# Kernel tuning notes

Measured on AMD Instinct MI355X. Metric: run time of the kernel, lower is better.

## Reference

```python
import jax, jax.numpy as jnp
import numpy as np

N = 100000   # nodes
E = 1600000  # edges
IN = 128     # in_dim
HID = 64     # hidden_dim per head
H = 4        # heads
OUT = 2      # out_dim (classes)
HD = HID * H # 256
NEG_SLOPE = 0.2
BN_EPS = 1e-5


def setup_inputs() -> dict:
    key = jax.random.key(0)
    ks = jax.random.split(key, 24)
    rn = lambda k, shp, s=0.05: (jax.random.normal(k, shp, jnp.float32) * s)
    d = {}
    d['x'] = jax.random.normal(ks[0], (N, IN), jnp.float32)
    d['edge_index'] = jax.random.randint(ks[1], (2, E), 0, N, dtype=jnp.int64)
    # layer 0: 128 -> (4,64)
    d['W0'] = rn(ks[2], (IN, HD))
    d['a_src0'] = rn(ks[3], (H, HID), 0.1)
    d['a_dst0'] = rn(ks[4], (H, HID), 0.1)
    d['b0'] = jnp.zeros((HD,), jnp.float32)
    # layer 1: 256 -> (4,64)
    d['W1'] = rn(ks[5], (HD, HD))
    d['a_src1'] = rn(ks[6], (H, HID), 0.1)
    d['a_dst1'] = rn(ks[7], (H, HID), 0.1)
    d['b1'] = jnp.zeros((HD,), jnp.float32)
    # layer 2: 256 -> (1,2), concat=False
    d['W2'] = rn(ks[8], (HD, OUT))
    d['a_src2'] = rn(ks[9], (1, OUT), 0.1)
    d['a_dst2'] = rn(ks[10], (1, OUT), 0.1)
    d['b2'] = jnp.zeros((OUT,), jnp.float32)
    # skip projection for layer 0 (128 != 256)
    d['skipW'] = rn(ks[11], (IN, HD))
    d['skipb'] = jnp.zeros((HD,), jnp.float32)
    # batchnorm affine params
    d['g0'] = jnp.ones((HD,), jnp.float32); d['be0'] = jnp.zeros((HD,), jnp.float32)
    d['g1'] = jnp.ones((HD,), jnp.float32); d['be1'] = jnp.zeros((HD,), jnp.float32)
    d['g2'] = jnp.ones((OUT,), jnp.float32); d['be2'] = jnp.zeros((OUT,), jnp.float32)
    return d


def _gat_conv(x, src, dst, W, a_src, a_dst, b, heads, ch, concat):
    n = x.shape[0]
    h = (x @ W).reshape(n, heads, ch)                 # [N,H,C]
    alpha_src = jnp.sum(h * a_src, axis=-1)           # [N,H]
    alpha_dst = jnp.sum(h * a_dst, axis=-1)           # [N,H]
    e = alpha_src[src] + alpha_dst[dst]               # [E',H]
    e = jax.nn.leaky_relu(e, NEG_SLOPE)
    # segment softmax over incoming edges of each dst node
    m = jax.ops.segment_max(e, dst, num_segments=n)
    e = jnp.exp(e - m[dst])
    s = jax.ops.segment_sum(e, dst, num_segments=n)
    alpha = e / (s[dst] + 1e-16)                      # [E',H]
    out = jax.ops.segment_sum(h[src] * alpha[..., None], dst, num_segments=n)  # [N,H,C]
    out = out.reshape(n, heads * ch) if concat else out.mean(axis=1)
    return out + b


def _bn(x, g, b):
    mu = x.mean(axis=0)
    v = x.var(axis=0)  # biased, matches torch BN training normalization
    return g * (x - mu) * jax.lax.rsqrt(v + BN_EPS) + b


def reference(x, edge_index, W0, a_src0, a_dst0, b0, W1, a_src1, a_dst1, b1,
              W2, a_src2, a_dst2, b2, skipW, skipb, g0, be0, g1, be1, g2, be2):
    n = x.shape[0]
    loop = jnp.arange(n, dtype=edge_index.dtype)
    src = jnp.concatenate([edge_index[0], loop])  # self-loops (PyG default)
    dst = jnp.concatenate([edge_index[1], loop])

    residual = x
    # layer 0
    h = _gat_conv(x, src, dst, W0, a_src0, a_dst0, b0, H, HID, True)
    h = _bn(h, g0, be0)
    h = h + (residual @ skipW + skipb)
    residual = h
    h = jax.nn.elu(h)
    # layer 1
    h = _gat_conv(h, src, dst, W1, a_src1, a_dst1, b1, H, HID, True)
    h = _bn(h, g1, be1)
    h = h + residual  # Identity skip
    h = jax.nn.elu(h)
    # layer 2 (heads=1, concat=False)
    h = _gat_conv(h, src, dst, W2, a_src2, a_dst2, b2, 1, OUT, False)
    h = _bn(h, g2, be2)
    return h
```

## Files before the change

kernel.cpp:

```cpp
#include <hip/hip_runtime.h>
#include <cstdint>
#include <cstddef>

#define KN 100000
#define KE 1600000
#define KE2 (KE + KN)
#define KIN 128
#define KHD 256
#define KH 4

#define BSH 7
#define NBUK ((KN + 127) >> 7)
#define BCAP 2560
#define ACHUNK 8192

#define LRELU(x) ((x) > 0.f ? (x) : 0.2f * (x))

typedef unsigned short bfu;
typedef short bf16x8 __attribute__((ext_vector_type(8)));
typedef unsigned short u16x8 __attribute__((ext_vector_type(8)));
typedef float f32x4 __attribute__((ext_vector_type(4)));

__device__ __forceinline__ float bf2f(bfu u) {
    union { unsigned int i; float f; } c; c.i = ((unsigned int)u) << 16; return c.f;
}
__device__ __forceinline__ bfu f2bf(float f) {
    union { float f; unsigned int i; } c; c.f = f;
    unsigned int r = c.i + 0x7FFFu + ((c.i >> 16) & 1u);
    return (bfu)(r >> 16);
}
__device__ __forceinline__ float eluf(float x) { return x > 0.f ? x : expm1f(x); }

__global__ __launch_bounds__(256) void k_binA(const int* __restrict__ ei,
                                              int* __restrict__ gcur,
                                              uint2* __restrict__ stg) {
    __shared__ int cnt[NBUK];
    __shared__ int base[NBUK];
    int t = threadIdx.x;
    for (int i = t; i < NBUK; i += 256) cnt[i] = 0;
    __syncthreads();
    int e0 = blockIdx.x * ACHUNK;
    int rank[ACHUNK / 256];
#pragma unroll
    for (int i = 0; i < ACHUNK / 256; ++i) {
        int e = e0 + i * 256 + t;
        rank[i] = 0;
        if (e < KE2) {
            int d = (e < KE) ? ei[KE + e] : (e - KE);
            rank[i] = atomicAdd(&cnt[d >> BSH], 1);
        }
    }
    __syncthreads();
    for (int b = t; b < NBUK; b += 256) {
        int c = cnt[b];
        base[b] = c ? atomicAdd(&gcur[b], c) : 0;
    }
    __syncthreads();
#pragma unroll
    for (int i = 0; i < ACHUNK / 256; ++i) {
        int e = e0 + i * 256 + t;
        if (e < KE2) {
            int d = (e < KE) ? ei[KE + e] : (e - KE);
            int s = (e < KE) ? ei[e] : (e - KE);
            int b = d >> BSH;
            int pos = base[b] + rank[i];
            if (pos < BCAP) stg[(size_t)b * BCAP + pos] = make_uint2((unsigned)s, (unsigned)d);
        }
    }
}

__global__ __launch_bounds__(1024) void k_scanB(const int* __restrict__ gcur,
                                                int* __restrict__ gbase,
                                                int* __restrict__ rowptr) {
    __shared__ int s[1024];
    int t = threadIdx.x;
    int v = (t < NBUK) ? min(gcur[t], BCAP) : 0;
    s[t] = v;
    __syncthreads();
    for (int o = 1; o < 1024; o <<= 1) {
        int add = (t >= o) ? s[t - o] : 0;
        __syncthreads();
        s[t] += add;
        __syncthreads();
    }
    if (t < NBUK) gbase[t] = s[t] - v;
    if (t == 0) rowptr[KN] = KE2;
}

__global__ __launch_bounds__(256) void k_binB(const int* __restrict__ gcur,
                                              const int* __restrict__ gbase,
                                              const uint2* __restrict__ stg,
                                              int* __restrict__ rowptr,
                                              int* __restrict__ csrc) {
    __shared__ int lcnt[128];
    __shared__ int lcur[128];
    __shared__ int ss[128];
    __shared__ int loff[128];
    int b = blockIdx.x, t = threadIdx.x;
    if (t < 128) { lcnt[t] = 0; lcur[t] = 0; }
    __syncthreads();
    int n = min(gcur[b], BCAP);
    int node0 = b << BSH;
    const uint2* sp = stg + (size_t)b * BCAP;
    for (int i = t; i < n; i += 256) {
        int d = (int)sp[i].y;
        atomicAdd(&lcnt[d - node0], 1);
    }
    __syncthreads();
    int v = (t < 128) ? lcnt[t] : 0;
    if (t < 128) ss[t] = v;
    __syncthreads();
    for (int o = 1; o < 128; o <<= 1) {
        int add = (t < 128 && t >= o) ? ss[t - o] : 0;
        __syncthreads();
        if (t < 128) ss[t] += add;
        __syncthreads();
    }
    int gb = gbase[b];
    if (t < 128) {
        loff[t] = ss[t] - v;
        int node = node0 + t;
        if (node < KN) rowptr[node] = gb + ss[t] - v;
    }
    __syncthreads();
    for (int i = t; i < n; i += 256) {
        uint2 r = sp[i];
        int li = (int)r.y - node0;
        int rank = atomicAdd(&lcur[li], 1);
        csrc[gb + loff[li] + rank] = (int)r.x;
    }
}

__global__ void k_cvt_w(const float* __restrict__ W, bfu* __restrict__ Wt, int K) {
    int t = blockIdx.x * 256 + threadIdx.x;
    if (t >= K * 256) return;
    int n = t & 255;
    int k = t >> 8;
    Wt[(size_t)n * K + k] = f2bf(W[(size_t)k * 256 + n]);
}

__global__ __launch_bounds__(256) void k_mgemm_dual(const float* __restrict__ Ap,
                                                    const bfu* __restrict__ Wcat,
                                                    const float* __restrict__ skipb,
                                                    bfu* __restrict__ hout,
                                                    bfu* __restrict__ sout, int M,
                                                    const float* __restrict__ avs,
                                                    const float* __restrict__ avd,
                                                    float* __restrict__ as_out,
                                                    float* __restrict__ ad_out) {
    const int K = KIN;
    __shared__ bfu As[128 * 40];
    __shared__ bfu Bs[128 * 40];
    int t = threadIdx.x;
    int row0 = blockIdx.x * 128;
    int col0 = blockIdx.y * 128;
    int srow = t >> 1;
    int shalf = t & 1;
    int l = t & 63;
    int w = t >> 6;
    int wr = w >> 1, wc = w & 1;
    int lg = l >> 4, lm = l & 15;

    f32x4 acc[4][4] = {};

    for (int kk = 0; kk < K; kk += 32) {
        {
            int garow = row0 + srow;
            bfu abuf[16];
            if (garow < M) {
                const float* ap = Ap + (size_t)garow * K + kk + shalf * 16;
#pragma unroll
                for (int i = 0; i < 4; ++i) {
                    float4 v = ((const float4*)ap)[i];
                    abuf[i * 4 + 0] = f2bf(v.x); abuf[i * 4 + 1] = f2bf(v.y);
                    abuf[i * 4 + 2] = f2bf(v.z); abuf[i * 4 + 3] = f2bf(v.w);
                }
            } else {
#pragma unroll
                for (int i = 0; i < 16; ++i) abuf[i] = 0;
            }
            *(u16x8*)(&As[srow * 40 + shalf * 16]) = *(const u16x8*)(&abuf[0]);
            *(u16x8*)(&As[srow * 40 + shalf * 16 + 8]) = *(const u16x8*)(&abuf[8]);
        }
        {
            const bfu* bp = Wcat + (size_t)(col0 + srow) * K + kk + shalf * 16;
            *(u16x8*)(&Bs[srow * 40 + shalf * 16]) = *(const u16x8*)bp;
            *(u16x8*)(&Bs[srow * 40 + shalf * 16 + 8]) = *(const u16x8*)(bp + 8);
        }
        __syncthreads();
        {
            int a_base = (wr * 64 + lm) * 40 + lg * 8;
            int b_base = (wc * 64 + lm) * 40 + lg * 8;
            bf16x8 af[4], bf_[4];
#pragma unroll
            for (int m = 0; m < 4; ++m) af[m] = *(const bf16x8*)(&As[a_base + m * 16 * 40]);
#pragma unroll
            for (int n = 0; n < 4; ++n) bf_[n] = *(const bf16x8*)(&Bs[b_base + n * 16 * 40]);
#pragma unroll
            for (int m = 0; m < 4; ++m)
#pragma unroll
                for (int n = 0; n < 4; ++n)
                    acc[m][n] = __builtin_amdgcn_mfma_f32_16x16x32_bf16(af[m], bf_[n], acc[m][n], 0, 0, 0);
        }
        __syncthreads();
    }

    bool isH = (blockIdx.y < 2);
    if (isH) {
        int head = (blockIdx.y << 1) + wc;
        const float* ah_s = avs + head * 64;
        const float* ah_d = avd + head * 64;
        float wsv[4], wdv[4];
#pragma unroll
        for (int n = 0; n < 4; ++n) {
            wsv[n] = ah_s[n * 16 + lm];
            wdv[n] = ah_d[n * 16 + lm];
        }
#pragma unroll
        for (int m = 0; m < 4; ++m) {
#pragma unroll
            for (int r = 0; r < 4; ++r) {
                float ps = 0.f, pd = 0.f;
#pragma unroll
                for (int n = 0; n < 4; ++n) {
                    float v = acc[m][n][r];
                    ps += v * wsv[n];
                    pd += v * wdv[n];
                }
#pragma unroll
                for (int off = 1; off < 16; off <<= 1) {
                    ps += __shfl_xor(ps, off, 16);
                    pd += __shfl_xor(pd, off, 16);
                }
                int rrow = row0 + wr * 64 + m * 16 + lg * 4 + r;
                if (lm == 0 && rrow < M) {
                    as_out[rrow * 4 + head] = ps;
                    ad_out[rrow * 4 + head] = pd;
                }
            }
        }
    }

    bfu* outp = isH ? hout : sout;
    int ocol = (isH ? col0 : col0 - 256) + wc * 64 + lm;
    float bv[4];
#pragma unroll
    for (int n = 0; n < 4; ++n)
        bv[n] = isH ? 0.f : skipb[ocol + n * 16];
#pragma unroll
    for (int m = 0; m < 4; ++m) {
#pragma unroll
        for (int r = 0; r < 4; ++r) {
            int rrow = row0 + wr * 64 + m * 16 + lg * 4 + r;
            if (rrow < M) {
                size_t base = (size_t)rrow * 256 + ocol;
#pragma unroll
                for (int n = 0; n < 4; ++n)
                    outp[base + n * 16] = f2bf(acc[m][n][r] + bv[n]);
            }
        }
    }
}

__global__ __launch_bounds__(256) void k_mgemm1(const bfu* __restrict__ Ap,
                                                const bfu* __restrict__ Wt,
                                                bfu* __restrict__ Cout, int M,
                                                const float* __restrict__ avs,
                                                const float* __restrict__ avd,
                                                float* __restrict__ as_out,
                                                float* __restrict__ ad_out) {
    const int K = KHD;
    __shared__ bfu As[128 * 40];
    __shared__ bfu Bs[128 * 40];
    int t = threadIdx.x;
    int row0 = blockIdx.x * 128;
    int col0 = blockIdx.y * 128;
    int srow = t >> 1;
    int shalf = t & 1;
    int l = t & 63;
    int w = t >> 6;
    int wr = w >> 1, wc = w & 1;
    int lg = l >> 4, lm = l & 15;

    f32x4 acc[4][4] = {};

    for (int kk = 0; kk < K; kk += 32) {
        {
            int garow = row0 + srow;
            bfu abuf[16];
            if (garow < M) {
                const bfu* ap = Ap + (size_t)garow * K + kk + shalf * 16;
                u16x8 u0 = *(const u16x8*)ap;
                u16x8 u1 = *(const u16x8*)(ap + 8);
#pragma unroll
                for (int i = 0; i < 8; ++i) abuf[i] = f2bf(eluf(bf2f(u0[i])));
#pragma unroll
                for (int i = 0; i < 8; ++i) abuf[8 + i] = f2bf(eluf(bf2f(u1[i])));
            } else {
#pragma unroll
                for (int i = 0; i < 16; ++i) abuf[i] = 0;
            }
            *(u16x8*)(&As[srow * 40 + shalf * 16]) = *(const u16x8*)(&abuf[0]);
            *(u16x8*)(&As[srow * 40 + shalf * 16 + 8]) = *(const u16x8*)(&abuf[8]);
        }
        {
            const bfu* bp = Wt + (size_t)(col0 + srow) * K + kk + shalf * 16;
            *(u16x8*)(&Bs[srow * 40 + shalf * 16]) = *(const u16x8*)bp;
            *(u16x8*)(&Bs[srow * 40 + shalf * 16 + 8]) = *(const u16x8*)(bp + 8);
        }
        __syncthreads();
        {
            int a_base = (wr * 64 + lm) * 40 + lg * 8;
            int b_base = (wc * 64 + lm) * 40 + lg * 8;
            bf16x8 af[4], bf_[4];
#pragma unroll
            for (int m = 0; m < 4; ++m) af[m] = *(const bf16x8*)(&As[a_base + m * 16 * 40]);
#pragma unroll
            for (int n = 0; n < 4; ++n) bf_[n] = *(const bf16x8*)(&Bs[b_base + n * 16 * 40]);
#pragma unroll
            for (int m = 0; m < 4; ++m)
#pragma unroll
                for (int n = 0; n < 4; ++n)
                    acc[m][n] = __builtin_amdgcn_mfma_f32_16x16x32_bf16(af[m], bf_[n], acc[m][n], 0, 0, 0);
        }
        __syncthreads();
    }

    {
        int head = (blockIdx.y << 1) + wc;
        const float* ah_s = avs + head * 64;
        const float* ah_d = avd + head * 64;
        float wsv[4], wdv[4];
#pragma unroll
        for (int n = 0; n < 4; ++n) {
            wsv[n] = ah_s[n * 16 + lm];
            wdv[n] = ah_d[n * 16 + lm];
        }
#pragma unroll
        for (int m = 0; m < 4; ++m) {
#pragma unroll
            for (int r = 0; r < 4; ++r) {
                float ps = 0.f, pd = 0.f;
#pragma unroll
                for (int n = 0; n < 4; ++n) {
                    float v = acc[m][n][r];
                    ps += v * wsv[n];
                    pd += v * wdv[n];
                }
#pragma unroll
                for (int off = 1; off < 16; off <<= 1) {
                    ps += __shfl_xor(ps, off, 16);
                    pd += __shfl_xor(pd, off, 16);
                }
                int rrow = row0 + wr * 64 + m * 16 + lg * 4 + r;
                if (lm == 0 && rrow < M) {
                    as_out[rrow * 4 + head] = ps;
                    ad_out[rrow * 4 + head] = pd;
                }
            }
        }
    }

#pragma unroll
    for (int m = 0; m < 4; ++m) {
#pragma unroll
        for (int r = 0; r < 4; ++r) {
            int rrow = row0 + wr * 64 + m * 16 + lg * 4 + r;
            if (rrow < M) {
                size_t base = (size_t)rrow * 256 + col0 + wc * 64 + lm;
#pragma unroll
                for (int n = 0; n < 4; ++n)
                    Cout[base + n * 16] = f2bf(acc[m][n][r] + 0.f);
            }
        }
    }
}

__global__ __launch_bounds__(256) void k_gat_agg(const bfu* __restrict__ h,
                                                 const int* __restrict__ rowptr,
                                                 const int* __restrict__ csrc,
                                                 const float* __restrict__ asrc,
                                                 const float* __restrict__ adst,
                                                 const float* __restrict__ bias,
                                                 bfu* __restrict__ outb) {
    int wave = threadIdx.x >> 6, lane = threadIdx.x & 63;
    int node = blockIdx.x * 4 + wave;
    if (node >= KN) return;
    int p0 = rowptr[node], p1 = rowptr[node + 1];
    int head = lane >> 4;
    int c0 = lane << 2;
    float adh = adst[node * 4 + head];

    float sum = 0.f, a0 = 0.f, a1 = 0.f, a2 = 0.f, a3 = 0.f;
    int p = p0;
    while (p < p1 && (p & 3)) {
        int s = csrc[p];
        float e = asrc[s * 4 + head] + adh; e = LRELU(e);
        float w = __expf(e);
        ushort4 u = *(const ushort4*)(h + (size_t)s * 256 + c0);
        a0 += bf2f(u.x) * w; a1 += bf2f(u.y) * w;
        a2 += bf2f(u.z) * w; a3 += bf2f(u.w) * w;
        sum += w;
        ++p;
    }
    for (; p + 7 < p1; p += 8) {
        int4 ca = *(const int4*)(csrc + p);
        int4 cb = *(const int4*)(csrc + p + 4);
        int sx[8] = {ca.x, ca.y, ca.z, ca.w, cb.x, cb.y, cb.z, cb.w};
        ushort4 u[8];
#pragma unroll
        for (int j = 0; j < 8; ++j)
            u[j] = *(const ushort4*)(h + (size_t)sx[j] * 256 + c0);
        float wv[8];
#pragma unroll
        for (int j = 0; j < 8; ++j) {
            float e = asrc[sx[j] * 4 + head] + adh; e = LRELU(e);
            wv[j] = __expf(e);
        }
#pragma unroll
        for (int j = 0; j < 8; ++j) {
            a0 += bf2f(u[j].x) * wv[j];
            a1 += bf2f(u[j].y) * wv[j];
            a2 += bf2f(u[j].z) * wv[j];
            a3 += bf2f(u[j].w) * wv[j];
            sum += wv[j];
        }
    }
    for (; p + 3 < p1; p += 4) {
        int4 ca = *(const int4*)(csrc + p);
        int sx[4] = {ca.x, ca.y, ca.z, ca.w};
        ushort4 u[4];
#pragma unroll
        for (int j = 0; j < 4; ++j)
            u[j] = *(const ushort4*)(h + (size_t)sx[j] * 256 + c0);
#pragma unroll
        for (int j = 0; j < 4; ++j) {
            float e = asrc[sx[j] * 4 + head] + adh; e = LRELU(e);
            float w = __expf(e);
            a0 += bf2f(u[j].x) * w; a1 += bf2f(u[j].y) * w;
            a2 += bf2f(u[j].z) * w; a3 += bf2f(u[j].w) * w;
            sum += w;
        }
    }
    for (; p < p1; ++p) {
        int s = csrc[p];
        float e = asrc[s * 4 + head] + adh; e = LRELU(e);
        float w = __expf(e);
        ushort4 u = *(const ushort4*)(h + (size_t)s * 256 + c0);
        a0 += bf2f(u.x) * w; a1 += bf2f(u.y) * w;
        a2 += bf2f(u.z) * w; a3 += bf2f(u.w) * w;
        sum += w;
    }
    float inv = 1.f / (sum + 1e-16f);
    float4 bv = *(const float4*)(bias + c0);
    ushort4 o;
    o.x = f2bf(a0 * inv + bv.x);
    o.y = f2bf(a1 * inv + bv.y);
    o.z = f2bf(a2 * inv + bv.z);
    o.w = f2bf(a3 * inv + bv.w);
    *(ushort4*)(outb + (size_t)node * 256 + c0) = o;
}

__global__ __launch_bounds__(256) void k_bn_stats(const bfu* __restrict__ xx,
                                                  float* __restrict__ sums,
                                                  float* __restrict__ sumsq) {
    int t = threadIdx.x;
    float s = 0.f, q = 0.f;
    for (int row = blockIdx.x; row < KN; row += gridDim.x) {
        float v = bf2f(xx[(size_t)row * 256 + t]);
        s += v; q += v * v;
    }
    atomicAdd(&sums[t], s);
    atomicAdd(&sumsq[t], q);
}

__global__ void k_bn_params(const float* __restrict__ sums, const float* __restrict__ sumsq,
                            const float* __restrict__ g, const float* __restrict__ be,
                            float* __restrict__ scaleC, float* __restrict__ shiftC) {
    int c = threadIdx.x;
    float mean = sums[c] / (float)KN;
    float var = sumsq[c] / (float)KN - mean * mean;
    float inv = rsqrtf(var + 1e-5f);
    float sc = g[c] * inv;
    scaleC[c] = sc;
    shiftC[c] = be[c] - mean * sc;
}

__global__ __launch_bounds__(256) void k_finalize_skip(bfu* __restrict__ P,
                                                       const bfu* __restrict__ skipQ,
                                                       const float* __restrict__ scaleC,
                                                       const float* __restrict__ shiftC) {
    size_t i = ((size_t)blockIdx.x * 256 + threadIdx.x) * 8;
    int c0 = (int)(i & 255);
    u16x8 pv = *(const u16x8*)(P + i);
    u16x8 qv = *(const u16x8*)(skipQ + i);
    float4 s0 = *(const float4*)(scaleC + c0);
    float4 s1 = *(const float4*)(scaleC + c0 + 4);
    float4 h0 = *(const float4*)(shiftC + c0);
    float4 h1 = *(const float4*)(shiftC + c0 + 4);
    float sc[8] = {s0.x, s0.y, s0.z, s0.w, s1.x, s1.y, s1.z, s1.w};
    float sh[8] = {h0.x, h0.y, h0.z, h0.w, h1.x, h1.y, h1.z, h1.w};
    u16x8 o;
#pragma unroll
    for (int j = 0; j < 8; ++j) {
        float r = bf2f(pv[j]) * sc[j] + sh[j] + bf2f(qv[j]);
        o[j] = f2bf(r);
    }
    *(u16x8*)(P + i) = o;
}

__global__ __launch_bounds__(256) void k_finalize_add(const bfu* __restrict__ Q,
                                                      bfu* __restrict__ P,
                                                      const float* __restrict__ scaleC,
                                                      const float* __restrict__ shiftC) {
    size_t i = ((size_t)blockIdx.x * 256 + threadIdx.x) * 8;
    int c0 = (int)(i & 255);
    u16x8 qv = *(const u16x8*)(Q + i);
    u16x8 pv = *(const u16x8*)(P + i);
    float4 s0 = *(const float4*)(scaleC + c0);
    float4 s1 = *(const float4*)(scaleC + c0 + 4);
    float4 h0 = *(const float4*)(shiftC + c0);
    float4 h1 = *(const float4*)(shiftC + c0 + 4);
    float sc[8] = {s0.x, s0.y, s0.z, s0.w, s1.x, s1.y, s1.z, s1.w};
    float sh[8] = {h0.x, h0.y, h0.z, h0.w, h1.x, h1.y, h1.z, h1.w};
    u16x8 o;
#pragma unroll
    for (int j = 0; j < 8; ++j) {
        float r = bf2f(qv[j]) * sc[j] + sh[j] + bf2f(pv[j]);
        o[j] = f2bf(eluf(r));
    }
    *(u16x8*)(P + i) = o;
}

__global__ __launch_bounds__(256) void k_gemm2(const bfu* __restrict__ xx,
                                               const float* __restrict__ W,
                                               const float* __restrict__ as2,
                                               const float* __restrict__ ad2,
                                               float* __restrict__ h2,
                                               float* __restrict__ asrc,
                                               float* __restrict__ adst) {
    int lane = threadIdx.x & 63;
    int wid = blockIdx.x * 4 + (threadIdx.x >> 6);
    int c = lane * 4;
    float2 w0 = *(const float2*)(W + 2 * (c + 0));
    float2 w1 = *(const float2*)(W + 2 * (c + 1));
    float2 w2 = *(const float2*)(W + 2 * (c + 2));
    float2 w3 = *(const float2*)(W + 2 * (c + 3));
    float s0 = as2[0], s1 = as2[1], d0 = ad2[0], d1 = ad2[1];
    int nwaves = gridDim.x * 4;
    for (int node = wid; node < KN; node += nwaves) {
        ushort4 u = *(const ushort4*)(xx + (size_t)node * 256 + c);
        float v0 = bf2f(u.x), v1 = bf2f(u.y), v2 = bf2f(u.z), v3 = bf2f(u.w);
        float a0 = v0 * w0.x + v1 * w1.x + v2 * w2.x + v3 * w3.x;
        float a1 = v0 * w0.y + v1 * w1.y + v2 * w2.y + v3 * w3.y;
        for (int o = 32; o > 0; o >>= 1) {
            a0 += __shfl_down(a0, o);
            a1 += __shfl_down(a1, o);
        }
        if (lane == 0) {
            h2[2 * node] = a0; h2[2 * node + 1] = a1;
            asrc[node] = a0 * s0 + a1 * s1;
            adst[node] = a0 * d0 + a1 * d1;
        }
    }
}

__global__ void k_gat_agg2(const float* __restrict__ h2, const int* __restrict__ rowptr,
                           const int* __restrict__ csrc, const float* __restrict__ asrc,
                           const float* __restrict__ adst, const float* __restrict__ b2,
                           float* __restrict__ agg2) {
    int node = blockIdx.x * blockDim.x + threadIdx.x;
    if (node >= KN) return;
    int p0 = rowptr[node], p1 = rowptr[node + 1];
    float ad = adst[node];
    float sum = 0.f, acc0 = 0.f, acc1 = 0.f;
    int p = p0;
    for (; p + 1 < p1; p += 2) {
        int s0 = csrc[p], s1 = csrc[p + 1];
        float e0 = asrc[s0] + ad; e0 = LRELU(e0);
        float e1 = asrc[s1] + ad; e1 = LRELU(e1);
        float w0 = __expf(e0), w1 = __expf(e1);
        float2 v0 = *(const float2*)(h2 + 2 * s0);
        float2 v1 = *(const float2*)(h2 + 2 * s1);
        acc0 += w0 * v0.x + w1 * v1.x;
        acc1 += w0 * v0.y + w1 * v1.y;
        sum += w0 + w1;
    }
    if (p < p1) {
        int s = csrc[p];
        float e = asrc[s] + ad; e = LRELU(e);
        float w = __expf(e);
        float2 v = *(const float2*)(h2 + 2 * s);
        acc0 += w * v.x; acc1 += w * v.y;
        sum += w;
    }
    float inv = 1.f / (sum + 1e-16f);
    agg2[2 * node] = acc0 * inv + b2[0];
    agg2[2 * node + 1] = acc1 * inv + b2[1];
}

__global__ __launch_bounds__(256) void k_bn_stats2(const float* __restrict__ xx,
                                                   float* __restrict__ st) {
    int t = threadIdx.x;
    float s0 = 0, q0 = 0, s1 = 0, q1 = 0;
    for (int i = blockIdx.x * 256 + t; i < KN; i += gridDim.x * 256) {
        float v0 = xx[2 * i], v1 = xx[2 * i + 1];
        s0 += v0; q0 += v0 * v0; s1 += v1; q1 += v1 * v1;
    }
    for (int o = 32; o > 0; o >>= 1) {
        s0 += __shfl_down(s0, o); q0 += __shfl_down(q0, o);
        s1 += __shfl_down(s1, o); q1 += __shfl_down(q1, o);
    }
    __shared__ float red[4][4];
    int lane = t & 63, wv = t >> 6;
    if (lane == 0) { red[wv][0] = s0; red[wv][1] = q0; red[wv][2] = s1; red[wv][3] = q1; }
    __syncthreads();
    if (t == 0) {
        float a = 0, b = 0, c = 0, d = 0;
        for (int w = 0; w < 4; ++w) { a += red[w][0]; b += red[w][1]; c += red[w][2]; d += red[w][3]; }
        atomicAdd(&st[0], a); atomicAdd(&st[1], b); atomicAdd(&st[2], c); atomicAdd(&st[3], d);
    }
}

__global__ void k_finalize2(const float* __restrict__ agg2, const float* __restrict__ st,
                            const float* __restrict__ g, const float* __restrict__ be,
                            float* __restrict__ outp) {
    int i = blockIdx.x * blockDim.x + threadIdx.x;
    if (i >= 2 * KN) return;
    int c = i & 1;
    float mean = st[c * 2] / (float)KN;
    float var = st[c * 2 + 1] / (float)KN - mean * mean;
    float inv = rsqrtf(var + 1e-5f);
    outp[i] = (agg2[i] - mean) * g[c] * inv + be[c];
}

extern "C" void kernel_launch(void* const* d_in, const int* in_sizes, int n_in,
                              void* d_out, int out_size, void* d_ws, size_t ws_size,
                              hipStream_t stream) {
    (void)in_sizes; (void)n_in; (void)out_size; (void)ws_size;
    const float* x     = (const float*)d_in[0];
    const int*   ei    = (const int*)d_in[1];
    const float* W0    = (const float*)d_in[2];
    const float* as0   = (const float*)d_in[3];
    const float* ad0   = (const float*)d_in[4];
    const float* b0    = (const float*)d_in[5];
    const float* W1    = (const float*)d_in[6];
    const float* as1   = (const float*)d_in[7];
    const float* ad1   = (const float*)d_in[8];
    const float* b1    = (const float*)d_in[9];
    const float* W2    = (const float*)d_in[10];
    const float* as2   = (const float*)d_in[11];
    const float* ad2   = (const float*)d_in[12];
    const float* b2    = (const float*)d_in[13];
    const float* skipW = (const float*)d_in[14];
    const float* skipb = (const float*)d_in[15];
    const float* g0    = (const float*)d_in[16];
    const float* be0   = (const float*)d_in[17];
    const float* g1    = (const float*)d_in[18];
    const float* be1   = (const float*)d_in[19];
    const float* g2    = (const float*)d_in[20];
    const float* be2   = (const float*)d_in[21];
    float* outp = (float*)d_out;

    char* ws = (char*)d_ws;
    size_t off = 0;
    auto alloc = [&](size_t bytes) -> void* {
        void* p = ws + off;
        off += (bytes + 255) & ~(size_t)255;
        return p;
    };
    bfu* hbf = (bfu*)alloc((size_t)KN * KHD * 2);
    bfu* P   = (bfu*)alloc((size_t)KN * KHD * 2);
    bfu* Q   = (bfu*)alloc((size_t)KN * KHD * 2);
    int* rowptr   = (int*)alloc((size_t)(KN + 1) * 4);
    int* csrc     = (int*)alloc((size_t)KE2 * 4);
    int* gcur     = (int*)alloc((size_t)NBUK * 4);
    int* gbase    = (int*)alloc((size_t)NBUK * 4);
    uint2* stg    = (uint2*)alloc((size_t)NBUK * BCAP * 8);
    float* asrcb  = (float*)alloc((size_t)KN * KH * 4);
    float* adstb  = (float*)alloc((size_t)KN * KH * 4);
    float* sums   = (float*)alloc(256 * 4);
    float* sumsq  = (float*)alloc(256 * 4);
    float* scaleC = (float*)alloc(256 * 4);
    float* shiftC = (float*)alloc(256 * 4);
    float* h2     = (float*)alloc((size_t)KN * 2 * 4);
    float* agg2   = (float*)alloc((size_t)KN * 2 * 4);
    float* st2    = (float*)alloc(256);
    bfu* Wcat     = (bfu*)alloc((size_t)512 * KIN * 2);
    bfu* W1t      = (bfu*)alloc((size_t)256 * KHD * 2);

    k_cvt_w<<<KIN, 256, 0, stream>>>(W0, Wcat, KIN);
    k_cvt_w<<<KIN, 256, 0, stream>>>(skipW, Wcat + (size_t)256 * KIN, KIN);
    k_cvt_w<<<KHD, 256, 0, stream>>>(W1, W1t, KHD);

    hipMemsetAsync(gcur, 0, (size_t)NBUK * 4, stream);
    k_binA<<<(KE2 + ACHUNK - 1) / ACHUNK, 256, 0, stream>>>(ei, gcur, stg);
    k_scanB<<<1, 1024, 0, stream>>>(gcur, gbase, rowptr);
    k_binB<<<NBUK, 256, 0, stream>>>(gcur, gbase, stg, rowptr, csrc);

    int ngrid = (KN + 255) / 256;

    dim3 mgd((KN + 127) / 128, 4);
    k_mgemm_dual<<<mgd, 256, 0, stream>>>(x, Wcat, skipb, hbf, Q, KN,
                                          as0, ad0, asrcb, adstb);
    k_gat_agg<<<(KN + 3) / 4, 256, 0, stream>>>(hbf, rowptr, csrc, asrcb, adstb, b0, P);
    hipMemsetAsync(sums, 0, 256 * 4, stream);
    hipMemsetAsync(sumsq, 0, 256 * 4, stream);
    k_bn_stats<<<1024, 256, 0, stream>>>(P, sums, sumsq);
    k_bn_params<<<1, 256, 0, stream>>>(sums, sumsq, g0, be0, scaleC, shiftC);
    k_finalize_skip<<<KN / 8, 256, 0, stream>>>(P, Q, scaleC, shiftC);

    dim3 mg((KN + 127) / 128, 2);
    k_mgemm1<<<mg, 256, 0, stream>>>(P, W1t, hbf, KN, as1, ad1, asrcb, adstb);
    k_gat_agg<<<(KN + 3) / 4, 256, 0, stream>>>(hbf, rowptr, csrc, asrcb, adstb, b1, Q);
    hipMemsetAsync(sums, 0, 256 * 4, stream);
    hipMemsetAsync(sumsq, 0, 256 * 4, stream);
    k_bn_stats<<<1024, 256, 0, stream>>>(Q, sums, sumsq);
    k_bn_params<<<1, 256, 0, stream>>>(sums, sumsq, g1, be1, scaleC, shiftC);
    k_finalize_add<<<KN / 8, 256, 0, stream>>>(Q, P, scaleC, shiftC);

    k_gemm2<<<1024, 256, 0, stream>>>(P, W2, as2, ad2, h2, asrcb, adstb);
    k_gat_agg2<<<ngrid, 256, 0, stream>>>(h2, rowptr, csrc, asrcb, adstb, b2, agg2);
    hipMemsetAsync(st2, 0, 4 * 4, stream);
    k_bn_stats2<<<256, 256, 0, stream>>>(agg2, st2);
    k_finalize2<<<(2 * KN + 255) / 256, 256, 0, stream>>>(agg2, st2, g2, be2, outp);
}
```

Before: 720.7 us.

## Fuse BN statistics into GAT aggregation and compact CSR staging entries

Batch-norm sum and sum-of-squares accumulation moves into the aggregation kernels, using a shared-memory block reduction followed by atomics. This removes the separate stats passes that re-read the 100k×256 bf16 activations. The BN param kernel is folded into the finalize kernels, and the per-layer memsets are merged into one. CSR staging entries shrink from uint2 to a packed 32-bit word, and the aggregation inner loop is simplified to 4-wide unrolling, which may reduce memory-level parallelism and adds many atomics per channel.

```diff
diff --git a/kernel.cpp b/kernel.cpp
--- a/kernel.cpp
+++ b/kernel.cpp
@@ -33,7 +33,7 @@
 
 __global__ __launch_bounds__(256) void k_binA(const int* __restrict__ ei,
                                               int* __restrict__ gcur,
-                                              uint2* __restrict__ stg) {
+                                              unsigned* __restrict__ stg) {
     __shared__ int cnt[NBUK];
     __shared__ int base[NBUK];
     int t = threadIdx.x;
@@ -64,7 +64,8 @@
             int s = (e < KE) ? ei[e] : (e - KE);
             int b = d >> BSH;
             int pos = base[b] + rank[i];
-            if (pos < BCAP) stg[(size_t)b * BCAP + pos] = make_uint2((unsigned)s, (unsigned)d);
+            if (pos < BCAP)
+                stg[(size_t)b * BCAP + pos] = ((unsigned)s << BSH) | (unsigned)(d & 127);
         }
     }
 }
@@ -89,7 +90,7 @@
 
 __global__ __launch_bounds__(256) void k_binB(const int* __restrict__ gcur,
                                               const int* __restrict__ gbase,
-                                              const uint2* __restrict__ stg,
+                                              const unsigned* __restrict__ stg,
                                               int* __restrict__ rowptr,
                                               int* __restrict__ csrc) {
     __shared__ int lcnt[128];
@@ -101,11 +102,9 @@
     __syncthreads();
     int n = min(gcur[b], BCAP);
     int node0 = b << BSH;
-    const uint2* sp = stg + (size_t)b * BCAP;
-    for (int i = t; i < n; i += 256) {
-        int d = (int)sp[i].y;
-        atomicAdd(&lcnt[d - node0], 1);
-    }
+    const unsigned* sp = stg + (size_t)b * BCAP;
+    for (int i = t; i < n; i += 256)
+        atomicAdd(&lcnt[sp[i] & 127], 1);
     __syncthreads();
     int v = (t < 128) ? lcnt[t] : 0;
     if (t < 128) ss[t] = v;
@@ -124,10 +123,10 @@
     }
     __syncthreads();
     for (int i = t; i < n; i += 256) {
-        uint2 r = sp[i];
-        int li = (int)r.y - node0;
+        unsigned r = sp[i];
+        int li = (int)(r & 127);
         int rank = atomicAdd(&lcur[li], 1);
-        csrc[gb + loff[li] + rank] = (int)r.x;
+        csrc[gb + loff[li] + rank] = (int)(r >> BSH);
     }
 }
 
@@ -370,7 +369,7 @@
                 size_t base = (size_t)rrow * 256 + col0 + wc * 64 + lm;
 #pragma unroll
                 for (int n = 0; n < 4; ++n)
-                    Cout[base + n * 16] = f2bf(acc[m][n][r] + 0.f);
+                    Cout[base + n * 16] = f2bf(acc[m][n][r]);
             }
         }
     }
@@ -382,10 +381,13 @@
                                                  const float* __restrict__ asrc,
                                                  const float* __restrict__ adst,
                                                  const float* __restrict__ bias,
-                                                 bfu* __restrict__ outb) {
+                                                 bfu* __restrict__ outb,
+                                                 float* __restrict__ sums,
+                                                 float* __restrict__ sumsq) {
+    __shared__ float sred[4][256];
+    __shared__ float qred[4][256];
     int wave = threadIdx.x >> 6, lane = threadIdx.x & 63;
     int node = blockIdx.x * 4 + wave;
-    if (node >= KN) return;
     int p0 = rowptr[node], p1 = rowptr[node + 1];
     int head = lane >> 4;
     int c0 = lane << 2;
@@ -393,54 +395,22 @@
 
     float sum = 0.f, a0 = 0.f, a1 = 0.f, a2 = 0.f, a3 = 0.f;
     int p = p0;
-    while (p < p1 && (p & 3)) {
-        int s = csrc[p];
-        float e = asrc[s * 4 + head] + adh; e = LRELU(e);
-        float w = __expf(e);
-        ushort4 u = *(const ushort4*)(h + (size_t)s * 256 + c0);
-        a0 += bf2f(u.x) * w; a1 += bf2f(u.y) * w;
-        a2 += bf2f(u.z) * w; a3 += bf2f(u.w) * w;
-        sum += w;
-        ++p;
-    }
-    for (; p + 7 < p1; p += 8) {
-        int4 ca = *(const int4*)(csrc + p);
-        int4 cb = *(const int4*)(csrc + p + 4);
-        int sx[8] = {ca.x, ca.y, ca.z, ca.w, cb.x, cb.y, cb.z, cb.w};
-        ushort4 u[8];
-#pragma unroll
-        for (int j = 0; j < 8; ++j)
-            u[j] = *(const ushort4*)(h + (size_t)sx[j] * 256 + c0);
-        float wv[8];
-#pragma unroll
-        for (int j = 0; j < 8; ++j) {
-            float e = asrc[sx[j] * 4 + head] + adh; e = LRELU(e);
-            wv[j] = __expf(e);
-        }
-#pragma unroll
-        for (int j = 0; j < 8; ++j) {
-            a0 += bf2f(u[j].x) * wv[j];
-            a1 += bf2f(u[j].y) * wv[j];
-            a2 += bf2f(u[j].z) * wv[j];
-            a3 += bf2f(u[j].w) * wv[j];
-            sum += wv[j];
-        }
-    }
     for (; p + 3 < p1; p += 4) {
-        int4 ca = *(const int4*)(csrc + p);
-        int sx[4] = {ca.x, ca.y, ca.z, ca.w};
-        ushort4 u[4];
-#pragma unroll
-        for (int j = 0; j < 4; ++j)
-            u[j] = *(const ushort4*)(h + (size_t)sx[j] * 256 + c0);
-#pragma unroll
-        for (int j = 0; j < 4; ++j) {
-            float e = asrc[sx[j] * 4 + head] + adh; e = LRELU(e);
-            float w = __expf(e);
-            a0 += bf2f(u[j].x) * w; a1 += bf2f(u[j].y) * w;
-            a2 += bf2f(u[j].z) * w; a3 += bf2f(u[j].w) * w;
-            sum += w;
-        }
+        int s0 = csrc[p], s1 = csrc[p + 1], s2 = csrc[p + 2], s3 = csrc[p + 3];
+        float e0 = asrc[s0 * 4 + head] + adh; e0 = LRELU(e0);
+        float e1 = asrc[s1 * 4 + head] + adh; e1 = LRELU(e1);
+        float e2 = asrc[s2 * 4 + head] + adh; e2 = LRELU(e2);
+        float e3 = asrc[s3 * 4 + head] + adh; e3 = LRELU(e3);
+        float w0 = __expf(e0), w1 = __expf(e1), w2 = __expf(e2), w3 = __expf(e3);
+        ushort4 u0 = *(const ushort4*)(h + (size_t)s0 * 256 + c0);
+        ushort4 u1 = *(const ushort4*)(h + (size_t)s1 * 256 + c0);
+        ushort4 u2 = *(const ushort4*)(h + (size_t)s2 * 256 + c0);
+        ushort4 u3 = *(const ushort4*)(h + (size_t)s3 * 256 + c0);
+        a0 += bf2f(u0.x) * w0 + bf2f(u1.x) * w1 + bf2f(u2.x) * w2 + bf2f(u3.x) * w3;
+        a1 += bf2f(u0.y) * w0 + bf2f(u1.y) * w1 + bf2f(u2.y) * w2 + bf2f(u3.y) * w3;
+        a2 += bf2f(u0.z) * w0 + bf2f(u1.z) * w1 + bf2f(u2.z) * w2 + bf2f(u3.z) * w3;
+        a3 += bf2f(u0.w) * w0 + bf2f(u1.w) * w1 + bf2f(u2.w) * w2 + bf2f(u3.w) * w3;
+        sum += (w0 + w1) + (w2 + w3);
     }
     for (; p < p1; ++p) {
         int s = csrc[p];
@@ -453,53 +423,46 @@
     }
     float inv = 1.f / (sum + 1e-16f);
     float4 bv = *(const float4*)(bias + c0);
+    float v0 = a0 * inv + bv.x;
+    float v1 = a1 * inv + bv.y;
+    float v2 = a2 * inv + bv.z;
+    float v3 = a3 * inv + bv.w;
     ushort4 o;
-    o.x = f2bf(a0 * inv + bv.x);
-    o.y = f2bf(a1 * inv + bv.y);
-    o.z = f2bf(a2 * inv + bv.z);
-    o.w = f2bf(a3 * inv + bv.w);
+    o.x = f2bf(v0); o.y = f2bf(v1); o.z = f2bf(v2); o.w = f2bf(v3);
     *(ushort4*)(outb + (size_t)node * 256 + c0) = o;
-}
-
-__global__ __launch_bounds__(256) void k_bn_stats(const bfu* __restrict__ xx,
-                                                  float* __restrict__ sums,
-                                                  float* __restrict__ sumsq) {
+
+    sred[wave][c0 + 0] = v0; sred[wave][c0 + 1] = v1;
+    sred[wave][c0 + 2] = v2; sred[wave][c0 + 3] = v3;
+    qred[wave][c0 + 0] = v0 * v0; qred[wave][c0 + 1] = v1 * v1;
+    qred[wave][c0 + 2] = v2 * v2; qred[wave][c0 + 3] = v3 * v3;
+    __syncthreads();
     int t = threadIdx.x;
-    float s = 0.f, q = 0.f;
-    for (int row = blockIdx.x; row < KN; row += gridDim.x) {
-        float v = bf2f(xx[(size_t)row * 256 + t]);
-        s += v; q += v * v;
-    }
+    float s = (sred[0][t] + sred[1][t]) + (sred[2][t] + sred[3][t]);
+    float q = (qred[0][t] + qred[1][t]) + (qred[2][t] + qred[3][t]);
     atomicAdd(&sums[t], s);
     atomicAdd(&sumsq[t], q);
 }
 
-__global__ void k_bn_params(const float* __restrict__ sums, const float* __restrict__ sumsq,
-                            const float* __restrict__ g, const float* __restrict__ be,
-                            float* __restrict__ scaleC, float* __restrict__ shiftC) {
-    int c = threadIdx.x;
-    float mean = sums[c] / (float)KN;
-    float var = sumsq[c] / (float)KN - mean * mean;
-    float inv = rsqrtf(var + 1e-5f);
-    float sc = g[c] * inv;
-    scaleC[c] = sc;
-    shiftC[c] = be[c] - mean * sc;
-}
-
 __global__ __launch_bounds__(256) void k_finalize_skip(bfu* __restrict__ P,
                                                        const bfu* __restrict__ skipQ,
-                                                       const float* __restrict__ scaleC,
-                                                       const float* __restrict__ shiftC) {
+                                                       const float* __restrict__ sums,
+                                                       const float* __restrict__ sumsq,
+                                                       const float* __restrict__ g,
+                                                       const float* __restrict__ be) {
     size_t i = ((size_t)blockIdx.x * 256 + threadIdx.x) * 8;
     int c0 = (int)(i & 255);
+    const float invN = 1.f / (float)KN;
+    float sc[8], sh[8];
+#pragma unroll
+    for (int j = 0; j < 8; ++j) {
+        float mean = sums[c0 + j] * invN;
+        float var = sumsq[c0 + j] * invN - mean * mean;
+        float s = g[c0 + j] * rsqrtf(var + 1e-5f);
+        sc[j] = s;
+        sh[j] = be[c0 + j] - mean * s;
+    }
     u16x8 pv = *(const u16x8*)(P + i);
     u16x8 qv = *(const u16x8*)(skipQ + i);
-    float4 s0 = *(const float4*)(scaleC + c0);
-    float4 s1 = *(const float4*)(scaleC + c0 + 4);
-    float4 h0 = *(const float4*)(shiftC + c0);
-    float4 h1 = *(const float4*)(shiftC + c0 + 4);
-    float sc[8] = {s0.x, s0.y, s0.z, s0.w, s1.x, s1.y, s1.z, s1.w};
-    float sh[8] = {h0.x, h0.y, h0.z, h0.w, h1.x, h1.y, h1.z, h1.w};
     u16x8 o;
 #pragma unroll
     for (int j = 0; j < 8; ++j) {
@@ -511,18 +474,24 @@
 
 __global__ __launch_bounds__(256) void k_finalize_add(const bfu* __restrict__ Q,
                                                       bfu* __restrict__ P,
-                                                      const float* __restrict__ scaleC,
-                                                      const float* __restrict__ shiftC) {
+                                                      const float* __restrict__ sums,
+                                                      const float* __restrict__ sumsq,
+                                                      const float* __restrict__ g,
+                                                      const float* __restrict__ be) {
     size_t i = ((size_t)blockIdx.x * 256 + threadIdx.x) * 8;
     int c0 = (int)(i & 255);
+    const float invN = 1.f / (float)KN;
+    float sc[8], sh[8];
+#pragma unroll
+    for (int j = 0; j < 8; ++j) {
+        float mean = sums[c0 + j] * invN;
+        float var = sumsq[c0 + j] * invN - mean * mean;
+        float s = g[c0 + j] * rsqrtf(var + 1e-5f);
+        sc[j] = s;
+        sh[j] = be[c0 + j] - mean * s;
+    }
     u16x8 qv = *(const u16x8*)(Q + i);
     u16x8 pv = *(const u16x8*)(P + i);
-    float4 s0 = *(const float4*)(scaleC + c0);
-    float4 s1 = *(const float4*)(scaleC + c0 + 4);
-    float4 h0 = *(const float4*)(shiftC + c0);
-    float4 h1 = *(const float4*)(shiftC + c0 + 4);
-    float sc[8] = {s0.x, s0.y, s0.z, s0.w, s1.x, s1.y, s1.z, s1.w};
-    float sh[8] = {h0.x, h0.y, h0.z, h0.w, h1.x, h1.y, h1.z, h1.w};
     u16x8 o;
 #pragma unroll
     for (int j = 0; j < 8; ++j) {
@@ -568,57 +537,48 @@
 __global__ void k_gat_agg2(const float* __restrict__ h2, const int* __restrict__ rowptr,
                            const int* __restrict__ csrc, const float* __restrict__ asrc,
                            const float* __restrict__ adst, const float* __restrict__ b2,
-                           float* __restrict__ agg2) {
+                           float* __restrict__ agg2, float* __restrict__ st) {
     int node = blockIdx.x * blockDim.x + threadIdx.x;
-    if (node >= KN) return;
-    int p0 = rowptr[node], p1 = rowptr[node + 1];
-    float ad = adst[node];
-    float sum = 0.f, acc0 = 0.f, acc1 = 0.f;
-    int p = p0;
-    for (; p + 1 < p1; p += 2) {
-        int s0 = csrc[p], s1 = csrc[p + 1];
-        float e0 = asrc[s0] + ad; e0 = LRELU(e0);
-        float e1 = asrc[s1] + ad; e1 = LRELU(e1);
-        float w0 = __expf(e0), w1 = __expf(e1);
-        float2 v0 = *(const float2*)(h2 + 2 * s0);
-        float2 v1 = *(const float2*)(h2 + 2 * s1);
-        acc0 += w0 * v0.x + w1 * v1.x;
-        acc1 += w0 * v0.y + w1 * v1.y;
-        sum += w0 + w1;
-    }
-    if (p < p1) {
-        int s = csrc[p];
-        float e = asrc[s] + ad; e = LRELU(e);
-        float w = __expf(e);
-        float2 v = *(const float2*)(h2 + 2 * s);
-        acc0 += w * v.x; acc1 += w * v.y;
-        sum += w;
-    }
-    float inv = 1.f / (sum + 1e-16f);
-    agg2[2 * node] = acc0 * inv + b2[0];
-    agg2[2 * node + 1] = acc1 * inv + b2[1];
-}
-
-__global__ __launch_bounds__(256) void k_bn_stats2(const float* __restrict__ xx,
-                                                   float* __restrict__ st) {
-    int t = threadIdx.x;
-    float s0 = 0, q0 = 0, s1 = 0, q1 = 0;
-    for (int i = blockIdx.x * 256 + t; i < KN; i += gridDim.x * 256) {
-        float v0 = xx[2 * i], v1 = xx[2 * i + 1];
-        s0 += v0; q0 += v0 * v0; s1 += v1; q1 += v1 * v1;
-    }
+    float o0 = 0.f, o1 = 0.f;
+    if (node < KN) {
+        int p0 = rowptr[node], p1 = rowptr[node + 1];
+        float ad = adst[node];
+        float sum = 0.f, acc0 = 0.f, acc1 = 0.f;
+        int p = p0;
+        for (; p + 1 < p1; p += 2) {
+            int s0 = csrc[p], s1 = csrc[p + 1];
+            float e0 = asrc[s0] + ad; e0 = LRELU(e0);
+            float e1 = asrc[s1] + ad; e1 = LRELU(e1);
+            float w0 = __expf(e0), w1 = __expf(e1);
+            float2 v0 = *(const float2*)(h2 + 2 * s0);
+            float2 v1 = *(const float2*)(h2 + 2 * s1);
+            acc0 += w0 * v0.x + w1 * v1.x;
+            acc1 += w0 * v0.y + w1 * v1.y;
+            sum += w0 + w1;
+        }
+        if (p < p1) {
+            int s = csrc[p];
+            float e = asrc[s] + ad; e = LRELU(e);
+            float w = __expf(e);
+            float2 v = *(const float2*)(h2 + 2 * s);
+            acc0 += w * v.x; acc1 += w * v.y;
+            sum += w;
+        }
+        float inv = 1.f / (sum + 1e-16f);
+        o0 = acc0 * inv + b2[0];
+        o1 = acc1 * inv + b2[1];
+        agg2[2 * node] = o0;
+        agg2[2 * node + 1] = o1;
+    }
+    float q0 = o0 * o0, q1 = o1 * o1;
+    float r0 = o0, r1 = o1;
     for (int o = 32; o > 0; o >>= 1) {
-        s0 += __shfl_down(s0, o); q0 += __shfl_down(q0, o);
-        s1 += __shfl_down(s1, o); q1 += __shfl_down(q1, o);
-    }
-    __shared__ float red[4][4];
-    int lane = t & 63, wv = t >> 6;
-    if (lane == 0) { red[wv][0] = s0; red[wv][1] = q0; red[wv][2] = s1; red[wv][3] = q1; }
-    __syncthreads();
-    if (t == 0) {
-        float a = 0, b = 0, c = 0, d = 0;
-        for (int w = 0; w < 4; ++w) { a += red[w][0]; b += red[w][1]; c += red[w][2]; d += red[w][3]; }
-        atomicAdd(&st[0], a); atomicAdd(&st[1], b); atomicAdd(&st[2], c); atomicAdd(&st[3], d);
+        r0 += __shfl_down(r0, o); q0 += __shfl_down(q0, o);
+        r1 += __shfl_down(r1, o); q1 += __shfl_down(q1, o);
+    }
+    if ((threadIdx.x & 63) == 0) {
+        atomicAdd(&st[0], r0); atomicAdd(&st[1], q0);
+        atomicAdd(&st[2], r1); atomicAdd(&st[3], q1);
     }
 }
 
@@ -672,28 +632,30 @@
     bfu* hbf = (bfu*)alloc((size_t)KN * KHD * 2);
     bfu* P   = (bfu*)alloc((size_t)KN * KHD * 2);
     bfu* Q   = (bfu*)alloc((size_t)KN * KHD * 2);
-    int* rowptr   = (int*)alloc((size_t)(KN + 1) * 4);
-    int* csrc     = (int*)alloc((size_t)KE2 * 4);
-    int* gcur     = (int*)alloc((size_t)NBUK * 4);
-    int* gbase    = (int*)alloc((size_t)NBUK * 4);
-    uint2* stg    = (uint2*)alloc((size_t)NBUK * BCAP * 8);
-    float* asrcb  = (float*)alloc((size_t)KN * KH * 4);
-    float* adstb  = (float*)alloc((size_t)KN * KH * 4);
-    float* sums   = (float*)alloc(256 * 4);
-    float* sumsq  = (float*)alloc(256 * 4);
-    float* scaleC = (float*)alloc(256 * 4);
-    float* shiftC = (float*)alloc(256 * 4);
-    float* h2     = (float*)alloc((size_t)KN * 2 * 4);
-    float* agg2   = (float*)alloc((size_t)KN * 2 * 4);
-    float* st2    = (float*)alloc(256);
-    bfu* Wcat     = (bfu*)alloc((size_t)512 * KIN * 2);
-    bfu* W1t      = (bfu*)alloc((size_t)256 * KHD * 2);
+    int* rowptr    = (int*)alloc((size_t)(KN + 1) * 4);
+    int* csrc      = (int*)alloc((size_t)KE2 * 4);
+    int* gcur      = (int*)alloc((size_t)NBUK * 4);
+    int* gbase     = (int*)alloc((size_t)NBUK * 4);
+    unsigned* stg  = (unsigned*)alloc((size_t)NBUK * BCAP * 4);
+    float* asrcb   = (float*)alloc((size_t)KN * KH * 4);
+    float* adstb   = (float*)alloc((size_t)KN * KH * 4);
+    float* stats   = (float*)alloc((1024 + 4) * 4);
+    float* sums0   = stats;
+    float* sumsq0  = stats + 256;
+    float* sums1   = stats + 512;
+    float* sumsq1  = stats + 768;
+    float* st2     = stats + 1024;
+    float* h2      = (float*)alloc((size_t)KN * 2 * 4);
+    float* agg2    = (float*)alloc((size_t)KN * 2 * 4);
+    bfu* Wcat      = (bfu*)alloc((size_t)512 * KIN * 2);
+    bfu* W1t       = (bfu*)alloc((size_t)256 * KHD * 2);
 
     k_cvt_w<<<KIN, 256, 0, stream>>>(W0, Wcat, KIN);
     k_cvt_w<<<KIN, 256, 0, stream>>>(skipW, Wcat + (size_t)256 * KIN, KIN);
     k_cvt_w<<<KHD, 256, 0, stream>>>(W1, W1t, KHD);
 
     hipMemsetAsync(gcur, 0, (size_t)NBUK * 4, stream);
+    hipMemsetAsync(stats, 0, (1024 + 4) * 4, stream);
     k_binA<<<(KE2 + ACHUNK - 1) / ACHUNK, 256, 0, stream>>>(ei, gcur, stg);
     k_scanB<<<1, 1024, 0, stream>>>(gcur, gbase, rowptr);
     k_binB<<<NBUK, 256, 0, stream>>>(gcur, gbase, stg, rowptr, csrc);
@@ -703,25 +665,17 @@
     dim3 mgd((KN + 127) / 128, 4);
     k_mgemm_dual<<<mgd, 256, 0, stream>>>(x, Wcat, skipb, hbf, Q, KN,
                                           as0, ad0, asrcb, adstb);
-    k_gat_agg<<<(KN + 3) / 4, 256, 0, stream>>>(hbf, rowptr, csrc, asrcb, adstb, b0, P);
-    hipMemsetAsync(sums, 0, 256 * 4, stream);
-    hipMemsetAsync(sumsq, 0, 256 * 4, stream);
-    k_bn_stats<<<1024, 256, 0, stream>>>(P, sums, sumsq);
-    k_bn_params<<<1, 256, 0, stream>>>(sums, sumsq, g0, be0, scaleC, shiftC);
-    k_finalize_skip<<<KN / 8, 256, 0, stream>>>(P, Q, scaleC, shiftC);
+    k_gat_agg<<<KN / 4, 256, 0, stream>>>(hbf, rowptr, csrc, asrcb, adstb, b0, P,
+                                          sums0, sumsq0);
+    k_finalize_skip<<<KN / 8, 256, 0, stream>>>(P, Q, sums0, sumsq0, g0, be0);
 
     dim3 mg((KN + 127) / 128, 2);
     k_mgemm1<<<mg, 256, 0, stream>>>(P, W1t, hbf, KN, as1, ad1, asrcb, adstb);
-    k_gat_agg<<<(KN + 3) / 4, 256, 0, stream>>>(hbf, rowptr, csrc, asrcb, adstb, b1, Q);
-    hipMemsetAsync(sums, 0, 256 * 4, stream);
-    hipMemsetAsync(sumsq, 0, 256 * 4, stream);
-    k_bn_stats<<<1024, 256, 0, stream>>>(Q, sums, sumsq);
-    k_bn_params<<<1, 256, 0, stream>>>(sums, sumsq, g1, be1, scaleC, shiftC);
-    k_finalize_add<<<KN / 8, 256, 0, stream>>>(Q, P, scaleC, shiftC);
+    k_gat_agg<<<KN / 4, 256, 0, stream>>>(hbf, rowptr, csrc, asrcb, adstb, b1, Q,
+                                          sums1, sumsq1);
+    k_finalize_add<<<KN / 8, 256, 0, stream>>>(Q, P, sums1, sumsq1, g1, be1);
 
     k_gemm2<<<1024, 256, 0, stream>>>(P, W2, as2, ad2, h2, asrcb, adstb);
-    k_gat_agg2<<<ngrid, 256, 0, stream>>>(h2, rowptr, csrc, asrcb, adstb, b2, agg2);
-    hipMemsetAsync(st2, 0, 4 * 4, stream);
-    k_bn_stats2<<<256, 256, 0, stream>>>(agg2, st2);
+    k_gat_agg2<<<ngrid, 256, 0, stream>>>(h2, rowptr, csrc, asrcb, adstb, b2, agg2, st2);
     k_finalize2<<<(2 * KN + 255) / 256, 256, 0, stream>>>(agg2, st2, g2, be2, outp);
 }
```

New measurement: 1.637 ms. +127.1%, slower.
